# Kernel optimization log

Measured on AMD Instinct MI355X. Metric: run time of the kernel, lower is better.

## Reference

```python
import jax, jax.numpy as jnp
import numpy as np

D_MODEL = 1024
FFN = 4096
N_EXPERTS = 8
TOPK = 2
B, L = 4, 2048


def setup_inputs() -> dict:
    key = jax.random.key(0)
    ks = jax.random.split(key, 8)
    s_in = 1.0 / np.sqrt(D_MODEL)
    s_ffn = 1.0 / np.sqrt(FFN)
    x = jax.random.normal(ks[0], (B, L, D_MODEL), dtype=jnp.float32)
    gate_w = jax.random.uniform(ks[1], (D_MODEL, N_EXPERTS), jnp.float32, -s_in, s_in)
    gate_b = jax.random.uniform(ks[2], (N_EXPERTS,), jnp.float32, -s_in, s_in)
    w1 = jax.random.uniform(ks[3], (N_EXPERTS, D_MODEL, FFN), jnp.float32, -s_in, s_in)
    b1 = jax.random.uniform(ks[4], (N_EXPERTS, FFN), jnp.float32, -s_in, s_in)
    w2 = jax.random.uniform(ks[5], (N_EXPERTS, FFN, D_MODEL), jnp.float32, -s_ffn, s_ffn)
    b2 = jax.random.uniform(ks[6], (N_EXPERTS, D_MODEL), jnp.float32, -s_ffn, s_ffn)
    return {"x": x, "gate_w": gate_w, "gate_b": gate_b,
            "w1": w1, "b1": b1, "w2": w2, "b2": b2}


def _moe(x, gate_w, gate_b, w1, b1, w2, b2):
    bs, l, d = x.shape
    T = bs * l
    xf = x.reshape(T, d)                       # [T, D]
    # --- TopkRouter: sparse softmax over top-k gate logits ---
    logits = xf @ gate_w + gate_b              # [T, E]
    top_vals, top_idx = jax.lax.top_k(logits, TOPK)
    rows = jnp.arange(T)[:, None]
    sparse = jnp.full_like(logits, -jnp.inf).at[rows, top_idx].set(top_vals)
    gates = jax.nn.softmax(sparse, axis=-1)    # [T, E], zero for non-topk experts
    # --- per-expert FFN, combined with gate weights (gate==0 => no contribution,
    # identical math to the original masked gather/scatter loop, eval mode) ---
    out = jnp.zeros_like(xf)
    for e in range(N_EXPERTS):
        h = jax.nn.gelu(xf @ w1[e] + b1[e], approximate=False)  # exact GELU (torch default)
        y = h @ w2[e] + b2[e]
        out = out + gates[:, e:e + 1] * y
    return out.reshape(bs, l, d)


def reference(x, gate_w, gate_b, w1, b1, w2, b2):
    return _moe(x, gate_w, gate_b, w1, b1, w2, b2)
```

## Files before the change

kernel.cpp:

```cpp
#include <hip/hip_runtime.h>
#include <hip/hip_bf16.h>
#include <math.h>
#include <stdint.h>

#define T_TOKENS 8192
#define DM 1024
#define FFNDIM 4096
#define NE 8
#define CAP 8192

typedef __attribute__((ext_vector_type(8))) __bf16 bf16x8;
typedef __attribute__((ext_vector_type(4))) __bf16 bf16x4;
typedef __attribute__((ext_vector_type(4))) float f32x4;

__device__ __forceinline__ float gelu_exact(float v) {
    return 0.5f * v * (1.0f + erff(v * 0.70710678118654752440f));
}

union PK8 { __bf16 h[8]; uint4 v; };

__device__ __forceinline__ void gload16(const void* g, void* l) {
    __builtin_amdgcn_global_load_lds(
        (const __attribute__((address_space(1))) uint32_t*)g,
        (__attribute__((address_space(3))) uint32_t*)l, 16, 0, 0);
}

__global__ void zero_counts_kernel(int* __restrict__ counts) {
    if (threadIdx.x < NE) counts[threadIdx.x] = 0;
}

__global__ __launch_bounds__(256) void zero_out_kernel(float* __restrict__ out,
                                                       int* __restrict__ counts) {
    size_t i = (size_t)blockIdx.x * 256 + threadIdx.x;
    uint4 z = make_uint4(0u, 0u, 0u, 0u);
    uint4* p = (uint4*)out + i * 2;
    p[0] = z; p[1] = z;
    if (blockIdx.x == 0 && threadIdx.x < NE) counts[threadIdx.x] = 0;
}

__global__ __launch_bounds__(256) void transpose_cvt_kernel(
        const float* __restrict__ w, __bf16* __restrict__ wt, int K, int N) {
    __shared__ __bf16 tile[64][72];
    int ntb = blockIdx.x, ktb = blockIdx.y, e = blockIdx.z;
    const float* src = w + ((size_t)e * K + (size_t)ktb * 64) * N + ntb * 64;
    int t = threadIdx.x;
    int tx = t & 15, ty = t >> 4;
#pragma unroll
    for (int rr = 0; rr < 4; ++rr) {
        int r = ty + rr * 16;
        f32x4 v = *(const f32x4*)(src + (size_t)r * N + tx * 4);
#pragma unroll
        for (int j = 0; j < 4; ++j) tile[tx * 4 + j][r] = (__bf16)v[j];
    }
    __syncthreads();
    int ow = t & 7, oy = t >> 3;
#pragma unroll
    for (int rr = 0; rr < 2; ++rr) {
        int n = oy + rr * 32;
        uint4 val = *(const uint4*)&tile[n][ow * 8];
        *(uint4*)(wt + ((size_t)e * N + (size_t)ntb * 64 + n) * K
                  + (size_t)ktb * 64 + ow * 8) = val;
    }
}

__global__ __launch_bounds__(256) void router_kernel(
        const float* __restrict__ x, const float* __restrict__ gate_w,
        const float* __restrict__ gate_b, int* __restrict__ counts,
        int* __restrict__ idx_list, float* __restrict__ gate_list,
        uint32_t* __restrict__ pack) {
    int wave = threadIdx.x >> 6, lane = threadIdx.x & 63;
    int tk = blockIdx.x * 4 + wave;
    const float* xr = x + (size_t)tk * DM;
    float acc[NE];
#pragma unroll
    for (int e = 0; e < NE; ++e) acc[e] = 0.f;
#pragma unroll
    for (int i = 0; i < DM / 64; ++i) {
        int d = i * 64 + lane;
        float xv = xr[d];
        f32x4 g0v = *(const f32x4*)(gate_w + d * NE);
        f32x4 g1v = *(const f32x4*)(gate_w + d * NE + 4);
#pragma unroll
        for (int e = 0; e < 4; ++e) { acc[e] += xv * g0v[e]; acc[4 + e] += xv * g1v[e]; }
    }
#pragma unroll
    for (int e = 0; e < NE; ++e) {
#pragma unroll
        for (int m = 32; m > 0; m >>= 1) acc[e] += __shfl_xor(acc[e], m, 64);
    }
    if (lane == 0) {
        float v0 = -INFINITY, v1 = -INFINITY;
        int i0 = 0, i1 = 0;
#pragma unroll
        for (int e = 0; e < NE; ++e) {
            float l = acc[e] + gate_b[e];
            if (l > v0) { v1 = v0; i1 = i0; v0 = l; i0 = e; }
            else if (l > v1) { v1 = l; i1 = e; }
        }
        float g0 = 1.f / (1.f + expf(v1 - v0));
        float g1 = 1.f - g0;
        int p0 = atomicAdd(&counts[i0], 1);
        idx_list[i0 * CAP + p0] = tk;
        gate_list[i0 * CAP + p0] = g0;
        int p1 = atomicAdd(&counts[i1], 1);
        idx_list[i1 * CAP + p1] = tk;
        gate_list[i1 * CAP + p1] = g1;
        pack[tk] = ((uint32_t)((i0 << 13) | p0) << 16) | (uint32_t)((i1 << 13) | p1);
    }
}

__global__ void scan_kernel(const int* __restrict__ counts, int* __restrict__ pbase) {
    if (threadIdx.x == 0 && blockIdx.x == 0) {
        int s = 0;
        for (int e = 0; e < NE; ++e) { pbase[e] = s; s += (counts[e] + 127) & ~127; }
        pbase[NE] = s;
    }
}

__device__ __forceinline__ int find_expert(const int* pbase, int slot_tile) {
    int e = 0;
#pragma unroll
    for (int k = 0; k < NE - 1; ++k)
        if (pbase[k + 1] <= slot_tile) e = k + 1;
    return e;
}

__global__ __launch_bounds__(256, 4) void gemm1_kernel(
        const float* __restrict__ x, const __bf16* __restrict__ w1t,
        const float* __restrict__ b1, const int* __restrict__ counts,
        const int* __restrict__ pbase, const int* __restrict__ idx_list,
        __bf16* __restrict__ h, int chunk_start) {
    __shared__ __bf16 Alds[128 * 72];
    __shared__ __bf16 Blds[128 * 64];

    int nwg = gridDim.x;
    int wid = (blockIdx.x & 7) * (nwg >> 3) + (blockIdx.x >> 3);
    int MT  = nwg >> 5;
    int mtl = wid % MT;
    int nt  = wid / MT;

    int slot_tile = chunk_start + mtl * 128;
    if (slot_tile >= pbase[NE]) return;
    int e = find_expert(pbase, slot_tile);
    int cnt = counts[e];
    int loc_tile = slot_tile - pbase[e];
    if (loc_tile >= cnt) return;

    int t = threadIdx.x;
    int lane = t & 63, wave = t >> 6;

    int am = t >> 1, ahalf = (t & 1) * 32;
    int localc = loc_tile + am; if (localc > cnt - 1) localc = cnt - 1;
    int tok = idx_list[e * CAP + localc];
    const float* arow = x + (size_t)tok * DM + ahalf;
    __bf16* adst = Alds + am * 72 + ahalf;

    int brow_b = wave * 32 + (lane >> 3);
    int bchunk = lane & 7;
    const char* bsrc[4];
    char* bdst[4];
#pragma unroll
    for (int q = 0; q < 4; ++q) {
        int row = brow_b + q * 8;
        bsrc[q] = (const char*)(w1t + ((size_t)e * FFNDIM + nt * 128 + row) * DM)
                  + ((bchunk ^ (row & 7)) << 4);
        bdst[q] = (char*)Blds + (wave * 4 + q) * 1024;
    }

    int wm = (wave >> 1) * 64, wn = (wave & 1) * 64;
    int l15 = lane & 15, quad = lane >> 4;

    f32x4 acc[4][4];
#pragma unroll
    for (int i = 0; i < 4; ++i)
#pragma unroll
        for (int j = 0; j < 4; ++j) acc[i][j] = f32x4{0.f, 0.f, 0.f, 0.f};

    for (int kb = 0; kb < DM; kb += 64) {
        f32x4 av[8];
        const f32x4* ap = (const f32x4*)(arow + kb);
#pragma unroll
        for (int q = 0; q < 8; ++q) av[q] = ap[q];
        uint4 apk[4];
#pragma unroll
        for (int q = 0; q < 4; ++q) {
            PK8 u;
#pragma unroll
            for (int w = 0; w < 4; ++w) {
                u.h[w]     = (__bf16)av[2 * q][w];
                u.h[4 + w] = (__bf16)av[2 * q + 1][w];
            }
            apk[q] = u.v;
        }
        __syncthreads();
#pragma unroll
        for (int q = 0; q < 4; ++q) gload16(bsrc[q] + kb * 2, bdst[q]);
#pragma unroll
        for (int q = 0; q < 4; ++q) *(uint4*)(adst + q * 8) = apk[q];
        __syncthreads();
#pragma unroll
        for (int ks = 0; ks < 2; ++ks) {
            int ko = ks * 32 + quad * 8;
            int kc = ks * 4 + quad;
            bf16x8 af[4], bfr[4];
#pragma unroll
            for (int i = 0; i < 4; ++i)
                af[i] = *(const bf16x8*)(Alds + (wm + i * 16 + l15) * 72 + ko);
#pragma unroll
            for (int j = 0; j < 4; ++j) {
                int n = wn + j * 16 + l15;
                bfr[j] = *(const bf16x8*)(Blds + n * 64 + ((kc ^ (n & 7)) << 3));
            }
#pragma unroll
            for (int i = 0; i < 4; ++i)
#pragma unroll
                for (int j = 0; j < 4; ++j)
                    acc[i][j] = __builtin_amdgcn_mfma_f32_16x16x32_bf16(
                        af[i], bfr[j], acc[i][j], 0, 0, 0);
        }
    }
    float bias[4];
#pragma unroll
    for (int j = 0; j < 4; ++j)
        bias[j] = b1[(size_t)e * FFNDIM + nt * 128 + wn + j * 16 + l15];
#pragma unroll
    for (int i = 0; i < 4; ++i) {
#pragma unroll
        for (int r = 0; r < 4; ++r) {
            int rowl = wm + i * 16 + quad * 4 + r;
            if (loc_tile + rowl < cnt) {
                size_t hoff = (size_t)(mtl * 128 + rowl) * FFNDIM + nt * 128;
#pragma unroll
                for (int j = 0; j < 4; ++j) {
                    float v = acc[i][j][r] + bias[j];
                    h[hoff + wn + j * 16 + l15] = (__bf16)gelu_exact(v);
                }
            }
        }
    }
}

template<int YM>
__global__ __launch_bounds__(256, 4) void gemm2_kernel(
        const __bf16* __restrict__ h, const __bf16* __restrict__ w2t,
        const float* __restrict__ b2, const int* __restrict__ counts,
        const int* __restrict__ pbase, const int* __restrict__ idx_list,
        const float* __restrict__ gate_list, float* __restrict__ out,
        void* __restrict__ ybuf, int ksp_count, int chunk_start) {
    __shared__ __bf16 Alds[128 * 64];
    __shared__ __bf16 Blds[128 * 64];

    int nwg = gridDim.x;
    int wid = (blockIdx.x & 7) * (nwg >> 3) + (blockIdx.x >> 3);
    int MT  = nwg / (8 * ksp_count);
    int mtl = wid % MT;
    int nt  = (wid / MT) & 7;
    int ksp = wid / (MT * 8);
    int kspan = FFNDIM / ksp_count;

    int slot_tile = chunk_start + mtl * 128;
    if (slot_tile >= pbase[NE]) return;
    int e = find_expert(pbase, slot_tile);
    int cnt = counts[e];
    int loc_tile = slot_tile - pbase[e];
    if (loc_tile >= cnt) return;

    int t = threadIdx.x;
    int lane = t & 63, wave = t >> 6;

    int row_b = wave * 32 + (lane >> 3);
    int chnk = lane & 7;
    const char* asrc[4];
    const char* bsrc[4];
    char* adst[4];
    char* bdst[4];
#pragma unroll
    for (int q = 0; q < 4; ++q) {
        int row = row_b + q * 8;
        int sw = ((chnk ^ (row & 7)) << 4);
        asrc[q] = (const char*)(h + (size_t)(mtl * 128 + row) * FFNDIM
                                + (size_t)ksp * kspan) + sw;
        bsrc[q] = (const char*)(w2t + ((size_t)e * DM + nt * 128 + row) * FFNDIM
                                + (size_t)ksp * kspan) + sw;
        adst[q] = (char*)Alds + (wave * 4 + q) * 1024;
        bdst[q] = (char*)Blds + (wave * 4 + q) * 1024;
    }

    int wm = (wave >> 1) * 64, wn = (wave & 1) * 64;
    int l15 = lane & 15, quad = lane >> 4;

    f32x4 acc[4][4];
#pragma unroll
    for (int i = 0; i < 4; ++i)
#pragma unroll
        for (int j = 0; j < 4; ++j) acc[i][j] = f32x4{0.f, 0.f, 0.f, 0.f};

    for (int kb = 0; kb < kspan; kb += 64) {
        __syncthreads();
#pragma unroll
        for (int q = 0; q < 4; ++q) gload16(asrc[q] + kb * 2, adst[q]);
#pragma unroll
        for (int q = 0; q < 4; ++q) gload16(bsrc[q] + kb * 2, bdst[q]);
        __syncthreads();
#pragma unroll
        for (int ks = 0; ks < 2; ++ks) {
            int ko = ks * 32 + quad * 8;
            int kc = ks * 4 + quad;
            bf16x8 af[4], bfr[4];
#pragma unroll
            for (int i = 0; i < 4; ++i) {
                int m = wm + i * 16 + l15;
                af[i] = *(const bf16x8*)(Alds + m * 64 + ((kc ^ (m & 7)) << 3));
            }
#pragma unroll
            for (int j = 0; j < 4; ++j) {
                int n = wn + j * 16 + l15;
                bfr[j] = *(const bf16x8*)(Blds + n * 64 + ((kc ^ (n & 7)) << 3));
            }
#pragma unroll
            for (int i = 0; i < 4; ++i)
#pragma unroll
                for (int j = 0; j < 4; ++j)
                    acc[i][j] = __builtin_amdgcn_mfma_f32_16x16x32_bf16(
                        af[i], bfr[j], acc[i][j], 0, 0, 0);
        }
    }
    float b2v[4];
#pragma unroll
    for (int j = 0; j < 4; ++j)
        b2v[j] = b2[(size_t)e * DM + nt * 128 + wn + j * 16 + l15];
#pragma unroll
    for (int i = 0; i < 4; ++i) {
#pragma unroll
        for (int r = 0; r < 4; ++r) {
            int rowl = wm + i * 16 + quad * 4 + r;
            int local = loc_tile + rowl;
            if (local < cnt) {
                float g = gate_list[e * CAP + local];
                if (YM == 0) {
                    int tok = idx_list[e * CAP + local];
                    float* orow = out + (size_t)tok * DM + nt * 128;
#pragma unroll
                    for (int j = 0; j < 4; ++j) {
                        float v = acc[i][j][r];
                        if (ksp == 0) v += b2v[j];
                        atomicAdd(orow + wn + j * 16 + l15, g * v);
                    }
                } else {
                    size_t yoff = (size_t)(slot_tile + rowl) * DM + nt * 128;
                    if (YM == 1) {
                        float* yr = (float*)ybuf + yoff;
#pragma unroll
                        for (int j = 0; j < 4; ++j)
                            yr[wn + j * 16 + l15] = g * (acc[i][j][r] + b2v[j]);
                    } else {
                        __bf16* yr = (__bf16*)ybuf + yoff;
#pragma unroll
                        for (int j = 0; j < 4; ++j)
                            yr[wn + j * 16 + l15] = (__bf16)(g * (acc[i][j][r] + b2v[j]));
                    }
                }
            }
        }
    }
}

template<int YM>
__global__ __launch_bounds__(256) void combine_kernel(
        const void* __restrict__ ybuf, const uint32_t* __restrict__ pack,
        const int* __restrict__ pbase, float* __restrict__ out) {
    int tk = blockIdx.x;
    uint32_t pk = pack[tk];
    uint32_t a = pk >> 16, b = pk & 0xffffu;
    size_t sa = (size_t)pbase[a >> 13] + (a & 8191u);
    size_t sb = (size_t)pbase[b >> 13] + (b & 8191u);
    int d = threadIdx.x * 4;
    f32x4 vo;
    if (YM == 1) {
        const float* y = (const float*)ybuf;
        f32x4 va = *(const f32x4*)(y + sa * DM + d);
        f32x4 vb = *(const f32x4*)(y + sb * DM + d);
#pragma unroll
        for (int j = 0; j < 4; ++j) vo[j] = va[j] + vb[j];
    } else {
        const __bf16* y = (const __bf16*)ybuf;
        bf16x4 va = *(const bf16x4*)(y + sa * DM + d);
        bf16x4 vb = *(const bf16x4*)(y + sb * DM + d);
#pragma unroll
        for (int j = 0; j < 4; ++j) vo[j] = (float)va[j] + (float)vb[j];
    }
    *(f32x4*)(out + (size_t)tk * DM + d) = vo;
}

extern "C" void kernel_launch(void* const* d_in, const int* in_sizes, int n_in,
                              void* d_out, int out_size, void* d_ws, size_t ws_size,
                              hipStream_t stream) {
    const float* x      = (const float*)d_in[0];
    const float* gate_w = (const float*)d_in[1];
    const float* gate_b = (const float*)d_in[2];
    const float* w1     = (const float*)d_in[3];
    const float* b1     = (const float*)d_in[4];
    const float* w2     = (const float*)d_in[5];
    const float* b2     = (const float*)d_in[6];
    float* out = (float*)d_out;

    char* wsb = (char*)d_ws;
    int*      counts   = (int*)wsb;
    int*      pbase    = (int*)(wsb + 64);
    int*      idx_list = (int*)(wsb + 128);
    float*    gate_lst = (float*)(wsb + 128 + 262144);
    uint32_t* pack     = (uint32_t*)(wsb + 128 + 524288);
    const size_t FIXED = 557184;
    const size_t W_ELEMS = (size_t)NE * DM * FFNDIM;
    __bf16* w1t = (__bf16*)(wsb + FIXED);
    __bf16* w2t = w1t + W_ELEMS;
    char*   dyn = (char*)(w2t + W_ELEMS);
    const size_t DYNBASE = FIXED + 4 * W_ELEMS;
    size_t avail = ws_size > DYNBASE ? ws_size - DYNBASE : 0;

    const size_t YB32 = 17408ull * DM * 4;
    const size_t YB16 = 17408ull * DM * 2;
    int S, NCH, YM, KSP;
    if      (avail >= YB32 + 17408ull * 8192) { S = 17408; NCH = 1;  YM = 1; KSP = 1; }
    else if (avail >= YB32 + 4096ull * 8192)  { S = 4096;  NCH = 5;  YM = 1; KSP = 1; }
    else if (avail >= YB16 + 4096ull * 8192)  { S = 4096;  NCH = 5;  YM = 2; KSP = 1; }
    else if (avail >= YB16 + 2048ull * 8192)  { S = 2048;  NCH = 9;  YM = 2; KSP = 1; }
    else                                      { S = 512;   NCH = 34; YM = 0; KSP = 8; }
    char*   ybuf = dyn;
    __bf16* hbuf = (__bf16*)(dyn + (YM == 1 ? YB32 : YM == 2 ? YB16 : 0));

    transpose_cvt_kernel<<<dim3(FFNDIM / 64, DM / 64, NE), 256, 0, stream>>>(
        w1, w1t, DM, FFNDIM);
    transpose_cvt_kernel<<<dim3(DM / 64, FFNDIM / 64, NE), 256, 0, stream>>>(
        w2, w2t, FFNDIM, DM);
    if (YM) zero_counts_kernel<<<1, 64, 0, stream>>>(counts);
    else    zero_out_kernel<<<4096, 256, 0, stream>>>(out, counts);
    router_kernel<<<2048, 256, 0, stream>>>(x, gate_w, gate_b, counts, idx_list,
                                            gate_lst, pack);
    scan_kernel<<<1, 64, 0, stream>>>(counts, pbase);

    int MT = S / 128;
    for (int c = 0; c < NCH; ++c) {
        gemm1_kernel<<<dim3(MT * 32), 256, 0, stream>>>(x, w1t, b1, counts, pbase,
                                                        idx_list, hbuf, c * S);
        if (YM == 1)
            gemm2_kernel<1><<<dim3(MT * 8), 256, 0, stream>>>(
                hbuf, w2t, b2, counts, pbase, idx_list, gate_lst, out, ybuf, 1, c * S);
        else if (YM == 2)
            gemm2_kernel<2><<<dim3(MT * 8), 256, 0, stream>>>(
                hbuf, w2t, b2, counts, pbase, idx_list, gate_lst, out, ybuf, 1, c * S);
        else
            gemm2_kernel<0><<<dim3(MT * 8 * KSP), 256, 0, stream>>>(
                hbuf, w2t, b2, counts, pbase, idx_list, gate_lst, out, ybuf, KSP, c * S);
    }
    if (YM == 1)
        combine_kernel<1><<<dim3(T_TOKENS), 256, 0, stream>>>(ybuf, pack, pbase, out);
    else if (YM == 2)
        combine_kernel<2><<<dim3(T_TOKENS), 256, 0, stream>>>(ybuf, pack, pbase, out);
}
```

Baseline: 1.112 ms.

## Use 256x256 tiles with double-buffered async LDS loads and pre-converted bf16 x

Both expert GEMMs now use 512-thread workgroups computing 256x256 tiles with a K-step of 32. Loads go through double-buffered global_load_lds with an XOR swizzle, so the next tile is fetched while the current one is multiplied. x is converted to bf16 once in a new kernel, which lets gemm1 load A asynchronously instead of converting fp32 in registers every step. Expert segments are padded to 256 rows, the chunk sizes and the k-split fallback are changed, and a balanced XCD swizzle remaps block ids. In exchange the larger tiles raise register pressure, add padding waste per expert, and reduce the number of workgroups available to fill the GPU.

```diff
diff --git a/kernel.cpp b/kernel.cpp
--- a/kernel.cpp
+++ b/kernel.cpp
@@ -8,6 +8,7 @@
 #define FFNDIM 4096
 #define NE 8
 #define CAP 8192
+#define SMAX 18432
 
 typedef __attribute__((ext_vector_type(8))) __bf16 bf16x8;
 typedef __attribute__((ext_vector_type(4))) __bf16 bf16x4;
@@ -23,6 +24,14 @@
     __builtin_amdgcn_global_load_lds(
         (const __attribute__((address_space(1))) uint32_t*)g,
         (__attribute__((address_space(3))) uint32_t*)l, 16, 0, 0);
+}
+
+__device__ __forceinline__ int xcd_swz(int nwg) {
+    int orig = blockIdx.x;
+    int xcd = orig & 7, loc = orig >> 3;
+    int q = nwg >> 3, r = nwg & 7;
+    int base = (xcd < r) ? xcd * (q + 1) : r * (q + 1) + (xcd - r) * q;
+    return base + loc;
 }
 
 __global__ void zero_counts_kernel(int* __restrict__ counts) {
@@ -36,6 +45,17 @@
     uint4* p = (uint4*)out + i * 2;
     p[0] = z; p[1] = z;
     if (blockIdx.x == 0 && threadIdx.x < NE) counts[threadIdx.x] = 0;
+}
+
+__global__ __launch_bounds__(256) void cvt_x_kernel(const float* __restrict__ x,
+                                                    __bf16* __restrict__ xb) {
+    size_t i = ((size_t)blockIdx.x * 256 + threadIdx.x) * 8;
+    f32x4 a = *(const f32x4*)(x + i);
+    f32x4 b = *(const f32x4*)(x + i + 4);
+    PK8 u;
+#pragma unroll
+    for (int j = 0; j < 4; ++j) { u.h[j] = (__bf16)a[j]; u.h[4 + j] = (__bf16)b[j]; }
+    *(uint4*)(xb + i) = u.v;
 }
 
 __global__ __launch_bounds__(256) void transpose_cvt_kernel(
@@ -112,7 +132,7 @@
 __global__ void scan_kernel(const int* __restrict__ counts, int* __restrict__ pbase) {
     if (threadIdx.x == 0 && blockIdx.x == 0) {
         int s = 0;
-        for (int e = 0; e < NE; ++e) { pbase[e] = s; s += (counts[e] + 127) & ~127; }
+        for (int e = 0; e < NE; ++e) { pbase[e] = s; s += (counts[e] + 255) & ~255; }
         pbase[NE] = s;
     }
 }
@@ -125,115 +145,106 @@
     return e;
 }
 
-__global__ __launch_bounds__(256, 4) void gemm1_kernel(
-        const float* __restrict__ x, const __bf16* __restrict__ w1t,
+
+__global__ __launch_bounds__(512, 2) void gemm1_kernel(
+        const __bf16* __restrict__ xb, const __bf16* __restrict__ w1t,
         const float* __restrict__ b1, const int* __restrict__ counts,
         const int* __restrict__ pbase, const int* __restrict__ idx_list,
         __bf16* __restrict__ h, int chunk_start) {
-    __shared__ __bf16 Alds[128 * 72];
-    __shared__ __bf16 Blds[128 * 64];
-
-    int nwg = gridDim.x;
-    int wid = (blockIdx.x & 7) * (nwg >> 3) + (blockIdx.x >> 3);
-    int MT  = nwg >> 5;
-    int mtl = wid % MT;
-    int nt  = wid / MT;
-
-    int slot_tile = chunk_start + mtl * 128;
+    __shared__ __bf16 Al[2][256 * 32];
+    __shared__ __bf16 Bl[2][256 * 32];
+
+    int wid = xcd_swz(gridDim.x);
+    int mtl = wid >> 4, nt = wid & 15;
+
+    int slot_tile = chunk_start + mtl * 256;
     if (slot_tile >= pbase[NE]) return;
     int e = find_expert(pbase, slot_tile);
     int cnt = counts[e];
-    int loc_tile = slot_tile - pbase[e];
-    if (loc_tile >= cnt) return;
-
-    int t = threadIdx.x;
-    int lane = t & 63, wave = t >> 6;
-
-    int am = t >> 1, ahalf = (t & 1) * 32;
-    int localc = loc_tile + am; if (localc > cnt - 1) localc = cnt - 1;
-    int tok = idx_list[e * CAP + localc];
-    const float* arow = x + (size_t)tok * DM + ahalf;
-    __bf16* adst = Alds + am * 72 + ahalf;
-
-    int brow_b = wave * 32 + (lane >> 3);
-    int bchunk = lane & 7;
-    const char* bsrc[4];
-    char* bdst[4];
-#pragma unroll
-    for (int q = 0; q < 4; ++q) {
-        int row = brow_b + q * 8;
-        bsrc[q] = (const char*)(w1t + ((size_t)e * FFNDIM + nt * 128 + row) * DM)
-                  + ((bchunk ^ (row & 7)) << 4);
-        bdst[q] = (char*)Blds + (wave * 4 + q) * 1024;
-    }
-
-    int wm = (wave >> 1) * 64, wn = (wave & 1) * 64;
+    int loc = slot_tile - pbase[e];
+    if (loc >= cnt) return;
+
+    int t = threadIdx.x, lane = t & 63, wave = t >> 6;
+
+    const char* asrc[2];
+    const char* bsrc[2];
+    uint32_t dofs[2];
+#pragma unroll
+    for (int q = 0; q < 2; ++q) {
+        int row = (wave * 2 + q) * 16 + (lane >> 2);
+        int ch  = lane & 3;
+        int sw  = ((ch ^ ((row >> 1) & 3)) << 4);
+        int lc = loc + row; if (lc > cnt - 1) lc = cnt - 1;
+        int tok = idx_list[e * CAP + lc];
+        asrc[q] = (const char*)(xb + (size_t)tok * DM) + sw;
+        bsrc[q] = (const char*)(w1t + ((size_t)e * FFNDIM + nt * 256 + row) * DM) + sw;
+        dofs[q] = (uint32_t)(wave * 2 + q) * 1024;
+    }
+
+    int wr = wave >> 2, wc = wave & 3;
     int l15 = lane & 15, quad = lane >> 4;
 
-    f32x4 acc[4][4];
-#pragma unroll
-    for (int i = 0; i < 4; ++i)
+    f32x4 acc[8][4];
+#pragma unroll
+    for (int i = 0; i < 8; ++i)
 #pragma unroll
         for (int j = 0; j < 4; ++j) acc[i][j] = f32x4{0.f, 0.f, 0.f, 0.f};
 
-    for (int kb = 0; kb < DM; kb += 64) {
-        f32x4 av[8];
-        const f32x4* ap = (const f32x4*)(arow + kb);
-#pragma unroll
-        for (int q = 0; q < 8; ++q) av[q] = ap[q];
-        uint4 apk[4];
-#pragma unroll
-        for (int q = 0; q < 4; ++q) {
-            PK8 u;
-#pragma unroll
-            for (int w = 0; w < 4; ++w) {
-                u.h[w]     = (__bf16)av[2 * q][w];
-                u.h[4 + w] = (__bf16)av[2 * q + 1][w];
+#pragma unroll
+    for (int q = 0; q < 2; ++q) {
+        gload16(asrc[q], (char*)Al[0] + dofs[q]);
+        gload16(bsrc[q], (char*)Bl[0] + dofs[q]);
+    }
+    __syncthreads();
+
+    const int NSTEP = DM / 32;
+    for (int st = 0; st < NSTEP; ++st) {
+        int cur = st & 1;
+        if (st + 1 < NSTEP) {
+            int off = (st + 1) * 64;
+#pragma unroll
+            for (int q = 0; q < 2; ++q) {
+                gload16(asrc[q] + off, (char*)Al[cur ^ 1] + dofs[q]);
+                gload16(bsrc[q] + off, (char*)Bl[cur ^ 1] + dofs[q]);
             }
-            apk[q] = u.v;
-        }
+        }
+        const __bf16* A = Al[cur];
+        const __bf16* B = Bl[cur];
+        bf16x8 af[8], bfr[4];
+#pragma unroll
+        for (int i = 0; i < 8; ++i) {
+            int m = wr * 128 + i * 16 + l15;
+            af[i] = *(const bf16x8*)(A + m * 32 + ((quad ^ ((m >> 1) & 3)) << 3));
+        }
+#pragma unroll
+        for (int j = 0; j < 4; ++j) {
+            int n = wc * 64 + j * 16 + l15;
+            bfr[j] = *(const bf16x8*)(B + n * 32 + ((quad ^ ((n >> 1) & 3)) << 3));
+        }
+#pragma unroll
+        for (int i = 0; i < 8; ++i)
+#pragma unroll
+            for (int j = 0; j < 4; ++j)
+                acc[i][j] = __builtin_amdgcn_mfma_f32_16x16x32_bf16(
+                    af[i], bfr[j], acc[i][j], 0, 0, 0);
         __syncthreads();
-#pragma unroll
-        for (int q = 0; q < 4; ++q) gload16(bsrc[q] + kb * 2, bdst[q]);
-#pragma unroll
-        for (int q = 0; q < 4; ++q) *(uint4*)(adst + q * 8) = apk[q];
-        __syncthreads();
-#pragma unroll
-        for (int ks = 0; ks < 2; ++ks) {
-            int ko = ks * 32 + quad * 8;
-            int kc = ks * 4 + quad;
-            bf16x8 af[4], bfr[4];
-#pragma unroll
-            for (int i = 0; i < 4; ++i)
-                af[i] = *(const bf16x8*)(Alds + (wm + i * 16 + l15) * 72 + ko);
-#pragma unroll
-            for (int j = 0; j < 4; ++j) {
-                int n = wn + j * 16 + l15;
-                bfr[j] = *(const bf16x8*)(Blds + n * 64 + ((kc ^ (n & 7)) << 3));
-            }
-#pragma unroll
-            for (int i = 0; i < 4; ++i)
-#pragma unroll
-                for (int j = 0; j < 4; ++j)
-                    acc[i][j] = __builtin_amdgcn_mfma_f32_16x16x32_bf16(
-                        af[i], bfr[j], acc[i][j], 0, 0, 0);
-        }
-    }
+    }
+
     float bias[4];
 #pragma unroll
     for (int j = 0; j < 4; ++j)
-        bias[j] = b1[(size_t)e * FFNDIM + nt * 128 + wn + j * 16 + l15];
-#pragma unroll
-    for (int i = 0; i < 4; ++i) {
+        bias[j] = b1[(size_t)e * FFNDIM + nt * 256 + wc * 64 + j * 16 + l15];
+#pragma unroll
+    for (int i = 0; i < 8; ++i) {
 #pragma unroll
         for (int r = 0; r < 4; ++r) {
-            int rowl = wm + i * 16 + quad * 4 + r;
-            if (loc_tile + rowl < cnt) {
-                size_t hoff = (size_t)(mtl * 128 + rowl) * FFNDIM + nt * 128;
+            int rowl = wr * 128 + i * 16 + quad * 4 + r;
+            if (loc + rowl < cnt) {
+                size_t hoff = (size_t)(mtl * 256 + rowl) * FFNDIM + nt * 256;
 #pragma unroll
                 for (int j = 0; j < 4; ++j) {
                     float v = acc[i][j][r] + bias[j];
-                    h[hoff + wn + j * 16 + l15] = (__bf16)gelu_exact(v);
+                    h[hoff + wc * 64 + j * 16 + l15] = (__bf16)gelu_exact(v);
                 }
             }
         }
@@ -241,123 +252,121 @@
 }
 
 template<int YM>
-__global__ __launch_bounds__(256, 4) void gemm2_kernel(
+__global__ __launch_bounds__(512, 2) void gemm2_kernel(
         const __bf16* __restrict__ h, const __bf16* __restrict__ w2t,
         const float* __restrict__ b2, const int* __restrict__ counts,
         const int* __restrict__ pbase, const int* __restrict__ idx_list,
         const float* __restrict__ gate_list, float* __restrict__ out,
-        void* __restrict__ ybuf, int ksp_count, int chunk_start) {
-    __shared__ __bf16 Alds[128 * 64];
-    __shared__ __bf16 Blds[128 * 64];
-
-    int nwg = gridDim.x;
-    int wid = (blockIdx.x & 7) * (nwg >> 3) + (blockIdx.x >> 3);
-    int MT  = nwg / (8 * ksp_count);
-    int mtl = wid % MT;
-    int nt  = (wid / MT) & 7;
-    int ksp = wid / (MT * 8);
-    int kspan = FFNDIM / ksp_count;
-
-    int slot_tile = chunk_start + mtl * 128;
+        void* __restrict__ ybuf, int chunk_start) {
+    __shared__ __bf16 Al[2][256 * 32];
+    __shared__ __bf16 Bl[2][256 * 32];
+
+    int wid = xcd_swz(gridDim.x);
+    int mtl = wid >> 2, nt = wid & 3;
+
+    int slot_tile = chunk_start + mtl * 256;
     if (slot_tile >= pbase[NE]) return;
     int e = find_expert(pbase, slot_tile);
     int cnt = counts[e];
-    int loc_tile = slot_tile - pbase[e];
-    if (loc_tile >= cnt) return;
-
-    int t = threadIdx.x;
-    int lane = t & 63, wave = t >> 6;
-
-    int row_b = wave * 32 + (lane >> 3);
-    int chnk = lane & 7;
-    const char* asrc[4];
-    const char* bsrc[4];
-    char* adst[4];
-    char* bdst[4];
-#pragma unroll
-    for (int q = 0; q < 4; ++q) {
-        int row = row_b + q * 8;
-        int sw = ((chnk ^ (row & 7)) << 4);
-        asrc[q] = (const char*)(h + (size_t)(mtl * 128 + row) * FFNDIM
-                                + (size_t)ksp * kspan) + sw;
-        bsrc[q] = (const char*)(w2t + ((size_t)e * DM + nt * 128 + row) * FFNDIM
-                                + (size_t)ksp * kspan) + sw;
-        adst[q] = (char*)Alds + (wave * 4 + q) * 1024;
-        bdst[q] = (char*)Blds + (wave * 4 + q) * 1024;
-    }
-
-    int wm = (wave >> 1) * 64, wn = (wave & 1) * 64;
+    int loc = slot_tile - pbase[e];
+    if (loc >= cnt) return;
+
+    int t = threadIdx.x, lane = t & 63, wave = t >> 6;
+
+    const char* asrc[2];
+    const char* bsrc[2];
+    uint32_t dofs[2];
+#pragma unroll
+    for (int q = 0; q < 2; ++q) {
+        int row = (wave * 2 + q) * 16 + (lane >> 2);
+        int ch  = lane & 3;
+        int sw  = ((ch ^ ((row >> 1) & 3)) << 4);
+        asrc[q] = (const char*)(h + (size_t)(mtl * 256 + row) * FFNDIM) + sw;
+        bsrc[q] = (const char*)(w2t + ((size_t)e * DM + nt * 256 + row) * FFNDIM) + sw;
+        dofs[q] = (uint32_t)(wave * 2 + q) * 1024;
+    }
+
+    int wr = wave >> 2, wc = wave & 3;
     int l15 = lane & 15, quad = lane >> 4;
 
-    f32x4 acc[4][4];
-#pragma unroll
-    for (int i = 0; i < 4; ++i)
+    f32x4 acc[8][4];
+#pragma unroll
+    for (int i = 0; i < 8; ++i)
 #pragma unroll
         for (int j = 0; j < 4; ++j) acc[i][j] = f32x4{0.f, 0.f, 0.f, 0.f};
 
-    for (int kb = 0; kb < kspan; kb += 64) {
+#pragma unroll
+    for (int q = 0; q < 2; ++q) {
+        gload16(asrc[q], (char*)Al[0] + dofs[q]);
+        gload16(bsrc[q], (char*)Bl[0] + dofs[q]);
+    }
+    __syncthreads();
+
+    const int NSTEP = FFNDIM / 32;
+    for (int st = 0; st < NSTEP; ++st) {
+        int cur = st & 1;
+        if (st + 1 < NSTEP) {
+            int off = (st + 1) * 64;
+#pragma unroll
+            for (int q = 0; q < 2; ++q) {
+                gload16(asrc[q] + off, (char*)Al[cur ^ 1] + dofs[q]);
+                gload16(bsrc[q] + off, (char*)Bl[cur ^ 1] + dofs[q]);
+            }
+        }
+        const __bf16* A = Al[cur];
+        const __bf16* B = Bl[cur];
+        bf16x8 af[8], bfr[4];
+#pragma unroll
+        for (int i = 0; i < 8; ++i) {
+            int m = wr * 128 + i * 16 + l15;
+            af[i] = *(const bf16x8*)(A + m * 32 + ((quad ^ ((m >> 1) & 3)) << 3));
+        }
+#pragma unroll
+        for (int j = 0; j < 4; ++j) {
+            int n = wc * 64 + j * 16 + l15;
+            bfr[j] = *(const bf16x8*)(B + n * 32 + ((quad ^ ((n >> 1) & 3)) << 3));
+        }
+#pragma unroll
+        for (int i = 0; i < 8; ++i)
+#pragma unroll
+            for (int j = 0; j < 4; ++j)
+                acc[i][j] = __builtin_amdgcn_mfma_f32_16x16x32_bf16(
+                    af[i], bfr[j], acc[i][j], 0, 0, 0);
         __syncthreads();
-#pragma unroll
-        for (int q = 0; q < 4; ++q) gload16(asrc[q] + kb * 2, adst[q]);
-#pragma unroll
-        for (int q = 0; q < 4; ++q) gload16(bsrc[q] + kb * 2, bdst[q]);
-        __syncthreads();
-#pragma unroll
-        for (int ks = 0; ks < 2; ++ks) {
-            int ko = ks * 32 + quad * 8;
-            int kc = ks * 4 + quad;
-            bf16x8 af[4], bfr[4];
-#pragma unroll
-            for (int i = 0; i < 4; ++i) {
-                int m = wm + i * 16 + l15;
-                af[i] = *(const bf16x8*)(Alds + m * 64 + ((kc ^ (m & 7)) << 3));
-            }
-#pragma unroll
-            for (int j = 0; j < 4; ++j) {
-                int n = wn + j * 16 + l15;
-                bfr[j] = *(const bf16x8*)(Blds + n * 64 + ((kc ^ (n & 7)) << 3));
-            }
-#pragma unroll
-            for (int i = 0; i < 4; ++i)
-#pragma unroll
-                for (int j = 0; j < 4; ++j)
-                    acc[i][j] = __builtin_amdgcn_mfma_f32_16x16x32_bf16(
-                        af[i], bfr[j], acc[i][j], 0, 0, 0);
-        }
-    }
+    }
+
     float b2v[4];
 #pragma unroll
     for (int j = 0; j < 4; ++j)
-        b2v[j] = b2[(size_t)e * DM + nt * 128 + wn + j * 16 + l15];
-#pragma unroll
-    for (int i = 0; i < 4; ++i) {
+        b2v[j] = b2[(size_t)e * DM + nt * 256 + wc * 64 + j * 16 + l15];
+#pragma unroll
+    for (int i = 0; i < 8; ++i) {
 #pragma unroll
         for (int r = 0; r < 4; ++r) {
-            int rowl = wm + i * 16 + quad * 4 + r;
-            int local = loc_tile + rowl;
+            int rowl = wr * 128 + i * 16 + quad * 4 + r;
+            int local = loc + rowl;
             if (local < cnt) {
                 float g = gate_list[e * CAP + local];
                 if (YM == 0) {
                     int tok = idx_list[e * CAP + local];
-                    float* orow = out + (size_t)tok * DM + nt * 128;
-#pragma unroll
-                    for (int j = 0; j < 4; ++j) {
-                        float v = acc[i][j][r];
-                        if (ksp == 0) v += b2v[j];
-                        atomicAdd(orow + wn + j * 16 + l15, g * v);
-                    }
+                    float* orow = out + (size_t)tok * DM + nt * 256;
+#pragma unroll
+                    for (int j = 0; j < 4; ++j)
+                        atomicAdd(orow + wc * 64 + j * 16 + l15,
+                                  g * (acc[i][j][r] + b2v[j]));
                 } else {
-                    size_t yoff = (size_t)(slot_tile + rowl) * DM + nt * 128;
+                    size_t yoff = (size_t)(slot_tile + rowl) * DM + nt * 256;
                     if (YM == 1) {
                         float* yr = (float*)ybuf + yoff;
 #pragma unroll
                         for (int j = 0; j < 4; ++j)
-                            yr[wn + j * 16 + l15] = g * (acc[i][j][r] + b2v[j]);
+                            yr[wc * 64 + j * 16 + l15] = g * (acc[i][j][r] + b2v[j]);
                     } else {
                         __bf16* yr = (__bf16*)ybuf + yoff;
 #pragma unroll
                         for (int j = 0; j < 4; ++j)
-                            yr[wn + j * 16 + l15] = (__bf16)(g * (acc[i][j][r] + b2v[j]));
+                            yr[wc * 64 + j * 16 + l15] =
+                                (__bf16)(g * (acc[i][j][r] + b2v[j]));
                     }
                 }
             }
@@ -414,21 +423,23 @@
     const size_t W_ELEMS = (size_t)NE * DM * FFNDIM;
     __bf16* w1t = (__bf16*)(wsb + FIXED);
     __bf16* w2t = w1t + W_ELEMS;
-    char*   dyn = (char*)(w2t + W_ELEMS);
-    const size_t DYNBASE = FIXED + 4 * W_ELEMS;
+    __bf16* xb  = w2t + W_ELEMS;
+    char*   dyn = (char*)(xb + (size_t)T_TOKENS * DM);
+    const size_t DYNBASE = FIXED + 4 * W_ELEMS + (size_t)T_TOKENS * DM * 2;
     size_t avail = ws_size > DYNBASE ? ws_size - DYNBASE : 0;
 
-    const size_t YB32 = 17408ull * DM * 4;
-    const size_t YB16 = 17408ull * DM * 2;
-    int S, NCH, YM, KSP;
-    if      (avail >= YB32 + 17408ull * 8192) { S = 17408; NCH = 1;  YM = 1; KSP = 1; }
-    else if (avail >= YB32 + 4096ull * 8192)  { S = 4096;  NCH = 5;  YM = 1; KSP = 1; }
-    else if (avail >= YB16 + 4096ull * 8192)  { S = 4096;  NCH = 5;  YM = 2; KSP = 1; }
-    else if (avail >= YB16 + 2048ull * 8192)  { S = 2048;  NCH = 9;  YM = 2; KSP = 1; }
-    else                                      { S = 512;   NCH = 34; YM = 0; KSP = 8; }
+    const size_t YB32 = (size_t)SMAX * DM * 4;
+    const size_t YB16 = (size_t)SMAX * DM * 2;
+    int S, NCH, YM;
+    if      (avail >= YB32 + 18432ull * 8192) { S = 18432; NCH = 1; YM = 1; }
+    else if (avail >= YB32 + 9216ull * 8192)  { S = 9216;  NCH = 2; YM = 1; }
+    else if (avail >= YB16 + 9216ull * 8192)  { S = 9216;  NCH = 2; YM = 2; }
+    else if (avail >= YB16 + 4608ull * 8192)  { S = 4608;  NCH = 4; YM = 2; }
+    else                                      { S = 2304;  NCH = 8; YM = 0; }
     char*   ybuf = dyn;
     __bf16* hbuf = (__bf16*)(dyn + (YM == 1 ? YB32 : YM == 2 ? YB16 : 0));
 
+    cvt_x_kernel<<<4096, 256, 0, stream>>>(x, xb);
     transpose_cvt_kernel<<<dim3(FFNDIM / 64, DM / 64, NE), 256, 0, stream>>>(
         w1, w1t, DM, FFNDIM);
     transpose_cvt_kernel<<<dim3(DM / 64, FFNDIM / 64, NE), 256, 0, stream>>>(
@@ -439,19 +450,19 @@
                                             gate_lst, pack);
     scan_kernel<<<1, 64, 0, stream>>>(counts, pbase);
 
-    int MT = S / 128;
+    int MT = S / 256;
     for (int c = 0; c < NCH; ++c) {
-        gemm1_kernel<<<dim3(MT * 32), 256, 0, stream>>>(x, w1t, b1, counts, pbase,
+        gemm1_kernel<<<dim3(MT * 16), 512, 0, stream>>>(xb, w1t, b1, counts, pbase,
                                                         idx_list, hbuf, c * S);
         if (YM == 1)
-            gemm2_kernel<1><<<dim3(MT * 8), 256, 0, stream>>>(
-                hbuf, w2t, b2, counts, pbase, idx_list, gate_lst, out, ybuf, 1, c * S);
+            gemm2_kernel<1><<<dim3(MT * 4), 512, 0, stream>>>(
+                hbuf, w2t, b2, counts, pbase, idx_list, gate_lst, out, ybuf, c * S);
         else if (YM == 2)
-            gemm2_kernel<2><<<dim3(MT * 8), 256, 0, stream>>>(
-                hbuf, w2t, b2, counts, pbase, idx_list, gate_lst, out, ybuf, 1, c * S);
+            gemm2_kernel<2><<<dim3(MT * 4), 512, 0, stream>>>(
+                hbuf, w2t, b2, counts, pbase, idx_list, gate_lst, out, ybuf, c * S);
         else
-            gemm2_kernel<0><<<dim3(MT * 8 * KSP), 256, 0, stream>>>(
-                hbuf, w2t, b2, counts, pbase, idx_list, gate_lst, out, ybuf, KSP, c * S);
+            gemm2_kernel<0><<<dim3(MT * 4), 512, 0, stream>>>(
+                hbuf, w2t, b2, counts, pbase, idx_list, gate_lst, out, ybuf, c * S);
     }
     if (YM == 1)
         combine_kernel<1><<<dim3(T_TOKENS), 256, 0, stream>>>(ybuf, pack, pbase, out);
```

New measurement: 1.265 ms. 13.7% more time.
